# Performance work log

Hardware: AMD Instinct MI355X
Metric: run time of the kernel (lower is better)

The kernel has to match this reference:

```python
import jax, jax.numpy as jnp
import numpy as np

B, N, C, D, O = 32, 512, 16, 256, 256


def setup_inputs() -> dict:
    key = jax.random.key(0)
    k1, k2, k3, k4, k5, k6 = jax.random.split(key, 6)
    std = 1.0 / np.sqrt(D)
    nodes = jax.random.normal(k1, (B, N, D), jnp.float32)
    children = jax.random.randint(k2, (B, N, C), 0, N)  # 0 == no-child sentinel
    w_t = jax.random.normal(k3, (D, O), jnp.float32) * std
    w_l = jax.random.normal(k4, (D, O), jnp.float32) * std
    w_r = jax.random.normal(k5, (D, O), jnp.float32) * std
    conv = jax.random.normal(k6, (O,), jnp.float32) * np.sqrt(2.0 / D)
    return {"nodes": nodes, "w_t": w_t, "w_l": w_l, "w_r": w_r, "conv": conv,
            "children": children}


def _coefs(children):
    # children: (B, N, C) int. Returns coef (B, N, C+1, 3) = stack(c_t, c_r, c_l).
    b, n, c = children.shape
    y = c + 1
    has_child = jnp.minimum(children, 1).astype(jnp.float32)          # (B,N,C)
    mask = jnp.concatenate([jnp.zeros((b, n, 1), jnp.float32), has_child], axis=2)  # (B,N,Y)
    # eta_t: 1 at slot 0 (parent), 0 elsewhere
    c_t = jnp.concatenate([jnp.ones((b, n, 1), jnp.float32),
                           jnp.zeros((b, n, c), jnp.float32)], axis=2)
    # eta_r
    ns = jnp.count_nonzero(children, axis=2).astype(jnp.float32)[..., None]  # (B,N,1)
    p = jnp.arange(-1.0, c, dtype=jnp.float32)                        # (Y,): -1,0,1,...
    child_idx = p * mask                                              # (B,N,Y)
    singles = (jnp.arange(y) == 1).astype(jnp.float32) * 0.5          # (Y,)
    denom = jnp.where(ns == 1.0, 1.0, ns - 1.0)                       # safe divide
    c_r = jnp.where(ns == 1.0,
                    jnp.broadcast_to(singles, mask.shape),
                    (1.0 - c_t) * (child_idx / denom))
    # eta_l
    c_l = (1.0 - c_t) * (1.0 - c_r) * mask
    return jnp.stack([c_t, c_r, c_l], axis=3)                         # (B,N,Y,3)


def reference(nodes, w_t, w_l, w_r, conv, children):
    b, n, d = nodes.shape
    c = children.shape[2]
    # gather children embeddings: child_emb[b,i,j] = nodes[b, children[b,i,j]]
    flat_idx = children.reshape(b, n * c)
    child_emb = jnp.take_along_axis(nodes, flat_idx[:, :, None], axis=1)
    child_emb = child_emb.reshape(b, n, c, d)
    child_emb = jnp.where((children == 0)[..., None], 0.0, child_emb)
    tree = jnp.concatenate([nodes[:, :, None, :], child_emb], axis=2)  # (B,N,Y,D)
    coef = _coefs(children)                                            # (B,N,Y,3)
    weights = jnp.stack([w_t, w_r, w_l], axis=0)                       # (3,D,O)
    agg = jnp.einsum('bnyd,bnyk->bnkd', tree, coef)                    # (B,N,3,D)
    res = jnp.einsum('bnkd,kdo->bno', agg, weights)                    # (B,N,O)
    return jax.nn.leaky_relu(res + conv, negative_slope=0.01)
```

## Files before the change

kernel.cpp:

```cpp
#include <hip/hip_runtime.h>
#include <hip/hip_bf16.h>
#include <stdint.h>

#define CC 16
#define OO 256
#define NSLAB 24
#define NB_ELS (16384 * 256)
#define A2STR 520

typedef __attribute__((ext_vector_type(8))) short bf16x8;
typedef __attribute__((ext_vector_type(4))) float f32x4;

__device__ __forceinline__ unsigned short f2bf(float x) {
    unsigned u = __builtin_bit_cast(unsigned, x);
    u += 0x7FFFu + ((u >> 16) & 1u);
    return (unsigned short)(u >> 16);
}

__global__ __launch_bounds__(256) void prep(
    const float* __restrict__ nodes, const float* __restrict__ wt,
    const float* __restrict__ wrp, const float* __restrict__ wl,
    unsigned short* __restrict__ nb, unsigned short* __restrict__ wsb) {

    __shared__ unsigned short T[256 * 40];
    const int p = blockIdx.x;
    const int tid = threadIdx.x;

    if (p < 2048) {
        const int pp = (p & 7) * 256 + (p >> 3);
        const size_t t = (size_t)pp * 256 + tid;
        const float4* s = (const float4*)nodes + t * 2;
        float4 a = s[0], b = s[1];
        uint4 u;
        u.x = (unsigned)f2bf(a.x) | ((unsigned)f2bf(a.y) << 16);
        u.y = (unsigned)f2bf(a.z) | ((unsigned)f2bf(a.w) << 16);
        u.z = (unsigned)f2bf(b.x) | ((unsigned)f2bf(b.y) << 16);
        u.w = (unsigned)f2bf(b.z) | ((unsigned)f2bf(b.w) << 16);
        *(uint4*)(nb + (t >> 5) * 256 + (t & 31) * 8) = u;
        return;
    }
    const int slab = p - 2048;
    const int n = tid;
#pragma unroll
    for (int kk = 0; kk < 32; ++kk) {
        const int k = slab * 32 + kk;
        const float* s = (k < 256) ? wt : ((k < 512) ? wrp : wl);
        T[n * 40 + kk] = f2bf(s[(k & 255) * OO + n]);
    }
    __syncthreads();
    uint4* dst = (uint4*)(wsb + slab * 8192 + n * 32);
    const uint4* src = (const uint4*)&T[n * 40];
#pragma unroll
    for (int q = 0; q < 4; ++q) dst[q] = src[q];
}

__global__ __launch_bounds__(256, 2) void tbcnn_fused(
    const int* __restrict__ children, const unsigned short* __restrict__ nb,
    const unsigned short* __restrict__ wsb, const float* __restrict__ conv,
    float* __restrict__ out) {

    __shared__ unsigned short A2[32 * A2STR];

    const int tid  = threadIdx.x;
    const int wave = tid >> 6;
    const int lane = tid & 63;
    const int x = blockIdx.x & 7;
    const int q = blockIdx.x >> 3;
    const int rbase = x * 2048 + q * 32;

#pragma unroll 2
    for (int i = 0; i < 8; ++i) {
        const int m  = wave * 8 + i;
        const int nf = __builtin_amdgcn_readfirstlane(rbase + m);
        const int brow = nf & ~511;
        const int* chp = children + (nf << 4);
        int cj[CC];
#pragma unroll
        for (int j = 0; j < CC; ++j) cj[j] = chp[j];
        int ns = 0;
#pragma unroll
        for (int j = 0; j < CC; ++j) ns += (cj[j] != 0) ? 1 : 0;
        const float inv_den = (ns > 1) ? 1.0f / (float)(ns - 1) : 0.0f;
        const bool single = (ns == 1);

        uint2 ec[CC];
#pragma unroll
        for (int j = 0; j < CC; ++j)
            ec[j] = *(const uint2*)(nb + (size_t)(brow + cj[j]) * 256 + lane * 4);

        float4 ar = make_float4(0.f, 0.f, 0.f, 0.f);
        float4 as = make_float4(0.f, 0.f, 0.f, 0.f);
#pragma unroll
        for (int j = 0; j < CC; ++j) {
            const float hasf = (cj[j] != 0) ? 1.0f : 0.0f;
            const float crr = single ? ((j == 0) ? 0.5f : 0.0f)
                                     : (float)j * inv_den;
            const float cr = crr * hasf;
            const float e0 = __builtin_bit_cast(float, ec[j].x << 16);
            const float e1 = __builtin_bit_cast(float, ec[j].x & 0xFFFF0000u);
            const float e2 = __builtin_bit_cast(float, ec[j].y << 16);
            const float e3 = __builtin_bit_cast(float, ec[j].y & 0xFFFF0000u);
            ar.x += cr * e0;   ar.y += cr * e1;   ar.z += cr * e2;   ar.w += cr * e3;
            as.x += hasf * e0; as.y += hasf * e1; as.z += hasf * e2; as.w += hasf * e3;
        }
        unsigned short* rowp = &A2[m * A2STR];
        uint2 v;
        v.x = (unsigned)f2bf(ar.x) | ((unsigned)f2bf(ar.y) << 16);
        v.y = (unsigned)f2bf(ar.z) | ((unsigned)f2bf(ar.w) << 16);
        *(uint2*)(rowp + lane * 4) = v;
        v.x = (unsigned)f2bf(as.x - ar.x) | ((unsigned)f2bf(as.y - ar.y) << 16);
        v.y = (unsigned)f2bf(as.z - ar.z) | ((unsigned)f2bf(as.w - ar.w) << 16);
        *(uint2*)(rowp + 256 + lane * 4) = v;
    }
    __syncthreads();

    const int quad = lane >> 4;
    const int l16  = lane & 15;
    f32x4 acc[2][4];
#pragma unroll
    for (int mi = 0; mi < 2; ++mi)
#pragma unroll
        for (int ni = 0; ni < 4; ++ni)
            acc[mi][ni] = (f32x4){0.f, 0.f, 0.f, 0.f};

    const unsigned short* bbase = wsb + (wave * 64 + l16) * 32 + quad * 8;
    const unsigned short* aG = nb + (size_t)(rbase + l16) * 256 + quad * 8;
    const unsigned short* aL = &A2[l16 * A2STR + quad * 8];

#pragma unroll 2
    for (int s = 0; s < 8; ++s) {
        bf16x8 af[2], bf[4];
        af[0] = *(const bf16x8*)(aG + s * 32);
        af[1] = *(const bf16x8*)(aG + 16 * 256 + s * 32);
#pragma unroll
        for (int ni = 0; ni < 4; ++ni)
            bf[ni] = *(const bf16x8*)(bbase + s * 8192 + ni * 512);
#pragma unroll
        for (int mi = 0; mi < 2; ++mi)
#pragma unroll
            for (int ni = 0; ni < 4; ++ni)
                acc[mi][ni] = __builtin_amdgcn_mfma_f32_16x16x32_bf16(
                    af[mi], bf[ni], acc[mi][ni], 0, 0, 0);
    }
#pragma unroll 2
    for (int s = 8; s < 24; ++s) {
        bf16x8 af[2], bf[4];
        af[0] = *(const bf16x8*)(aL + (s - 8) * 32);
        af[1] = *(const bf16x8*)(aL + 16 * A2STR + (s - 8) * 32);
#pragma unroll
        for (int ni = 0; ni < 4; ++ni)
            bf[ni] = *(const bf16x8*)(bbase + s * 8192 + ni * 512);
#pragma unroll
        for (int mi = 0; mi < 2; ++mi)
#pragma unroll
            for (int ni = 0; ni < 4; ++ni)
                acc[mi][ni] = __builtin_amdgcn_mfma_f32_16x16x32_bf16(
                    af[mi], bf[ni], acc[mi][ni], 0, 0, 0);
    }

#pragma unroll
    for (int ni = 0; ni < 4; ++ni) {
        const int col = wave * 64 + ni * 16 + l16;
        const float cv = conv[col];
#pragma unroll
        for (int mi = 0; mi < 2; ++mi) {
#pragma unroll
            for (int r = 0; r < 4; ++r) {
                const int row = rbase + mi * 16 + quad * 4 + r;
                float v = acc[mi][ni][r] + cv;
                v = (v > 0.f) ? v : 0.01f * v;
                out[(size_t)row * OO + col] = v;
            }
        }
    }
}

extern "C" void kernel_launch(void* const* d_in, const int* in_sizes, int n_in,
                              void* d_out, int out_size, void* d_ws, size_t ws_size,
                              hipStream_t stream) {
    const float* nodes    = (const float*)d_in[0];
    const float* w_t      = (const float*)d_in[1];
    const float* w_l      = (const float*)d_in[2];
    const float* w_r      = (const float*)d_in[3];
    const float* conv     = (const float*)d_in[4];
    const int*   children = (const int*)d_in[5];

    unsigned short* nb  = (unsigned short*)d_ws;
    unsigned short* wsb = nb + NB_ELS;

    prep<<<2048 + 24, 256, 0, stream>>>(nodes, w_t, w_r, w_l, nb, wsb);
    tbcnn_fused<<<512, 256, 0, stream>>>(children, nb, wsb, conv, (float*)d_out);
}
```

Before: 108.8 us.

## Split fused block work across 16 waves with smaller per-wave MFMA tiles

The block grows from 256 to 1024 threads. Each of 16 waves now builds 2 aggregated rows instead of 8 and computes a 16x32 output tile (2 accumulators) instead of 32x64. The aim is more latency hiding in the gather phase and more waves per CU. In exchange, per-wave data reuse drops: B fragments are reused across one A tile instead of two, so redundant global weight loads rise, and launch_bounds(1024,8) may limit registers.

```diff
diff --git a/kernel.cpp b/kernel.cpp
--- a/kernel.cpp
+++ b/kernel.cpp
@@ -54,7 +54,7 @@
     for (int q = 0; q < 4; ++q) dst[q] = src[q];
 }
 
-__global__ __launch_bounds__(256, 2) void tbcnn_fused(
+__global__ __launch_bounds__(1024, 8) void tbcnn_fused(
     const int* __restrict__ children, const unsigned short* __restrict__ nb,
     const unsigned short* __restrict__ wsb, const float* __restrict__ conv,
     float* __restrict__ out) {
@@ -68,9 +68,9 @@
     const int q = blockIdx.x >> 3;
     const int rbase = x * 2048 + q * 32;
 
-#pragma unroll 2
-    for (int i = 0; i < 8; ++i) {
-        const int m  = wave * 8 + i;
+#pragma unroll 1
+    for (int i = 0; i < 2; ++i) {
+        const int m  = wave * 2 + i;
         const int nf = __builtin_amdgcn_readfirstlane(rbase + m);
         const int brow = nf & ~511;
         const int* chp = children + (nf << 4);
@@ -116,61 +116,43 @@
 
     const int quad = lane >> 4;
     const int l16  = lane & 15;
-    f32x4 acc[2][4];
-#pragma unroll
-    for (int mi = 0; mi < 2; ++mi)
-#pragma unroll
-        for (int ni = 0; ni < 4; ++ni)
-            acc[mi][ni] = (f32x4){0.f, 0.f, 0.f, 0.f};
+    const int wr   = wave >> 3;
+    const int wc   = wave & 7;
+    f32x4 acc[2];
+    acc[0] = (f32x4){0.f, 0.f, 0.f, 0.f};
+    acc[1] = (f32x4){0.f, 0.f, 0.f, 0.f};
 
-    const unsigned short* bbase = wsb + (wave * 64 + l16) * 32 + quad * 8;
-    const unsigned short* aG = nb + (size_t)(rbase + l16) * 256 + quad * 8;
-    const unsigned short* aL = &A2[l16 * A2STR + quad * 8];
+    const unsigned short* bbase = wsb + (wc * 32 + l16) * 32 + quad * 8;
+    const unsigned short* aG = nb + (size_t)(rbase + wr * 16 + l16) * 256 + quad * 8;
+    const unsigned short* aL = &A2[(wr * 16 + l16) * A2STR + quad * 8];
 
 #pragma unroll 2
     for (int s = 0; s < 8; ++s) {
-        bf16x8 af[2], bf[4];
-        af[0] = *(const bf16x8*)(aG + s * 32);
-        af[1] = *(const bf16x8*)(aG + 16 * 256 + s * 32);
-#pragma unroll
-        for (int ni = 0; ni < 4; ++ni)
-            bf[ni] = *(const bf16x8*)(bbase + s * 8192 + ni * 512);
-#pragma unroll
-        for (int mi = 0; mi < 2; ++mi)
-#pragma unroll
-            for (int ni = 0; ni < 4; ++ni)
-                acc[mi][ni] = __builtin_amdgcn_mfma_f32_16x16x32_bf16(
-                    af[mi], bf[ni], acc[mi][ni], 0, 0, 0);
+        bf16x8 af = *(const bf16x8*)(aG + s * 32);
+        bf16x8 b0 = *(const bf16x8*)(bbase + s * 8192);
+        bf16x8 b1 = *(const bf16x8*)(bbase + s * 8192 + 512);
+        acc[0] = __builtin_amdgcn_mfma_f32_16x16x32_bf16(af, b0, acc[0], 0, 0, 0);
+        acc[1] = __builtin_amdgcn_mfma_f32_16x16x32_bf16(af, b1, acc[1], 0, 0, 0);
     }
 #pragma unroll 2
     for (int s = 8; s < 24; ++s) {
-        bf16x8 af[2], bf[4];
-        af[0] = *(const bf16x8*)(aL + (s - 8) * 32);
-        af[1] = *(const bf16x8*)(aL + 16 * A2STR + (s - 8) * 32);
-#pragma unroll
-        for (int ni = 0; ni < 4; ++ni)
-            bf[ni] = *(const bf16x8*)(bbase + s * 8192 + ni * 512);
-#pragma unroll
-        for (int mi = 0; mi < 2; ++mi)
-#pragma unroll
-            for (int ni = 0; ni < 4; ++ni)
-                acc[mi][ni] = __builtin_amdgcn_mfma_f32_16x16x32_bf16(
-                    af[mi], bf[ni], acc[mi][ni], 0, 0, 0);
+        bf16x8 af = *(const bf16x8*)(aL + (s - 8) * 32);
+        bf16x8 b0 = *(const bf16x8*)(bbase + s * 8192);
+        bf16x8 b1 = *(const bf16x8*)(bbase + s * 8192 + 512);
+        acc[0] = __builtin_amdgcn_mfma_f32_16x16x32_bf16(af, b0, acc[0], 0, 0, 0);
+        acc[1] = __builtin_amdgcn_mfma_f32_16x16x32_bf16(af, b1, acc[1], 0, 0, 0);
     }
 
 #pragma unroll
-    for (int ni = 0; ni < 4; ++ni) {
-        const int col = wave * 64 + ni * 16 + l16;
+    for (int ni = 0; ni < 2; ++ni) {
+        const int col = wc * 32 + ni * 16 + l16;
         const float cv = conv[col];
 #pragma unroll
-        for (int mi = 0; mi < 2; ++mi) {
-#pragma unroll
-            for (int r = 0; r < 4; ++r) {
-                const int row = rbase + mi * 16 + quad * 4 + r;
-                float v = acc[mi][ni][r] + cv;
-                v = (v > 0.f) ? v : 0.01f * v;
-                out[(size_t)row * OO + col] = v;
-            }
+        for (int r = 0; r < 4; ++r) {
+            const int row = rbase + wr * 16 + quad * 4 + r;
+            float v = acc[ni][r] + cv;
+            v = (v > 0.f) ? v : 0.01f * v;
+            out[(size_t)row * OO + col] = v;
         }
     }
 }
@@ -189,5 +171,5 @@
     unsigned short* wsb = nb + NB_ELS;
 
     prep<<<2048 + 24, 256, 0, stream>>>(nodes, w_t, w_r, w_l, nb, wsb);
-    tbcnn_fused<<<512, 256, 0, stream>>>(children, nb, wsb, conv, (float*)d_out);
+    tbcnn_fused<<<512, 1024, 0, stream>>>(children, nb, wsb, conv, (float*)d_out);
 }
```

New measurement: 117.8 us. 8.3% more time.
